# Kernel optimization log

Hardware: AMD Instinct MI355X
Metric: run time of the kernel (lower is better)

The kernel has to match this reference:

```python
import jax, jax.numpy as jnp
import numpy as np

HB, S, DK = 32, 2048, 128  # h*batch, seq_len, d_k
NEG = -1.0e9


def setup_inputs() -> dict:
    key = jax.random.key(0)
    kq, kk, kv = jax.random.split(key, 3)
    Q = jax.random.normal(kq, (HB, S, DK), dtype=jnp.float32)
    K = jax.random.normal(kk, (HB, S, DK), dtype=jnp.float32)
    V = jax.random.normal(kv, (HB, S, DK), dtype=jnp.float32)
    # causal mask, 1.0 where attending allowed, broadcast to all head*batch rows
    mask = jnp.broadcast_to(jnp.tril(jnp.ones((S, S), dtype=jnp.float32)), (HB, S, S))
    return {"Q": Q, "K": K, "V": V, "mask": mask}


def reference(Q, K, V, mask):
    d_k = Q.shape[-1]
    scores = jnp.einsum("bqd,bkd->bqk", Q, K) / jnp.sqrt(jnp.float32(d_k))
    scores = scores * mask + (1.0 - mask) * NEG
    p_attn = jax.nn.softmax(scores, axis=-1)
    # NOTE: original layer computes dropout(p_attn) but then discards it and
    # matmuls the un-dropped p_attn with V; we reproduce the inference math.
    out = jnp.einsum("bqk,bkd->bqd", p_attn, V)
    return (out, p_attn)
```

## Files before the change

kernel.cpp:

```cpp
#include <hip/hip_runtime.h>
#include <hip/hip_bf16.h>
#include <cstdint>

#define HB 32
#define SEQ 2048
#define DKDIM 128

typedef short s16x8 __attribute__((ext_vector_type(8)));
typedef float f32x4 __attribute__((ext_vector_type(4)));

__device__ __forceinline__ unsigned short f2bf(float x) {
  union { float f; uint32_t u; } v; v.f = x;
  uint32_t r = v.u + 0x7FFFu + ((v.u >> 16) & 1u);
  return (unsigned short)(r >> 16);
}
__device__ __forceinline__ float bf2f(unsigned short h) {
  union { uint32_t u; float f; } v; v.u = ((uint32_t)h) << 16;
  return v.f;
}

#define SCALE 0.08838834764831845f

__device__ __forceinline__ void barrier_lgkm_only() {
  asm volatile("s_waitcnt lgkmcnt(0)" ::: "memory");
  __builtin_amdgcn_s_barrier();
  __builtin_amdgcn_sched_barrier(0);
}

#define SK_KPAD 140
#define SK_KELEMS (64 * SK_KPAD)

__global__ __launch_bounds__(256, 4) void attn_sums(
    const float* __restrict__ Qg, const float* __restrict__ Kg, float* __restrict__ sums)
{
  __shared__ __align__(16) unsigned short K_lds[2 * SK_KELEMS];

  const int tid = threadIdx.x;
  const int lane = tid & 63;
  const int w = tid >> 6, g = lane >> 4, lr = lane & 15;
  const int b = blockIdx.y;
  const size_t bS = (size_t)b * SEQ;

  int x = blockIdx.x, qt = 0, acc = 0;
  for (;;) { int c = (qt >> 2) + 1; if (x < acc + c) break; acc += c; ++qt; }
  const int kc = x - acc;
  const int qb = qt << 6;
  const int t0 = kc << 2;
  const int nt = min(4, qt + 1 - t0);

  s16x8 qf[4];
  {
    const float* qrow = Qg + (bS + qb + w * 16 + lr) * DKDIM;
#pragma unroll
    for (int c = 0; c < 4; ++c) {
      const float* p = qrow + c * 32 + g * 8;
      float4 a = *(const float4*)p, bb = *(const float4*)(p + 4);
      s16x8 h;
      h[0] = (short)f2bf(a.x * SCALE); h[1] = (short)f2bf(a.y * SCALE);
      h[2] = (short)f2bf(a.z * SCALE); h[3] = (short)f2bf(a.w * SCALE);
      h[4] = (short)f2bf(bb.x * SCALE); h[5] = (short)f2bf(bb.y * SCALE);
      h[6] = (short)f2bf(bb.z * SCALE); h[7] = (short)f2bf(bb.w * SCALE);
      qf[c] = h;
    }
  }

  auto loadK = [&](int kt, float4* r) {
#pragma unroll
    for (int it = 0; it < 4; ++it) {
      int chunk = tid + (it << 8);
      const float* src = Kg + (bS + (kt << 6) + (chunk >> 4)) * (size_t)DKDIM + ((chunk & 15) << 3);
      r[2 * it] = *(const float4*)src;
      r[2 * it + 1] = *(const float4*)(src + 4);
    }
  };
  auto writeK = [&](unsigned short* dst, const float4* r) {
#pragma unroll
    for (int it = 0; it < 4; ++it) {
      int chunk = tid + (it << 8);
      int row = chunk >> 4, c8 = (chunk & 15) << 3;
      float4 a = r[2 * it], bb = r[2 * it + 1];
      s16x8 h;
      h[0] = (short)f2bf(a.x); h[1] = (short)f2bf(a.y); h[2] = (short)f2bf(a.z); h[3] = (short)f2bf(a.w);
      h[4] = (short)f2bf(bb.x); h[5] = (short)f2bf(bb.y); h[6] = (short)f2bf(bb.z); h[7] = (short)f2bf(bb.w);
      *(s16x8*)&dst[row * SK_KPAD + c8] = h;
    }
  };

  float4 kr[8];
  loadK(t0, kr);
  writeK(K_lds, kr);

  float rsum[4] = {0.f, 0.f, 0.f, 0.f};
  for (int j = 0; j < nt; ++j) {
    barrier_lgkm_only();
    const bool pf = (j + 1 < nt);
    if (pf) loadK(t0 + j + 1, kr);
    const unsigned short* Kb = K_lds + (j & 1) * SK_KELEMS;
    f32x4 sacc[4];
#pragma unroll
    for (int n = 0; n < 4; ++n) { f32x4 z = {0.f, 0.f, 0.f, 0.f}; sacc[n] = z; }
#pragma unroll
    for (int c = 0; c < 4; ++c)
#pragma unroll
      for (int n = 0; n < 4; ++n) {
        s16x8 bf = *(const s16x8*)&Kb[(n * 16 + lr) * SK_KPAD + (c << 5) + (g << 3)];
        sacc[n] = __builtin_amdgcn_mfma_f32_16x16x32_bf16(qf[c], bf, sacc[n], 0, 0, 0);
      }
    const int kt = t0 + j;
    if (kt == qt) {
#pragma unroll
      for (int n = 0; n < 4; ++n)
#pragma unroll
        for (int r = 0; r < 4; ++r) {
          const bool ok = ((kt << 6) + n * 16 + lr) <= (qb + w * 16 + g * 4 + r);
          rsum[r] += ok ? __expf(sacc[n][r]) : 0.0f;
        }
    } else {
#pragma unroll
      for (int n = 0; n < 4; ++n)
#pragma unroll
        for (int r = 0; r < 4; ++r) rsum[r] += __expf(sacc[n][r]);
    }
    if (pf) writeK(K_lds + ((j + 1) & 1) * SK_KELEMS, kr);
  }

#pragma unroll
  for (int r = 0; r < 4; ++r) {
    float v = rsum[r];
    v += __shfl_xor(v, 1, 64);
    v += __shfl_xor(v, 2, 64);
    v += __shfl_xor(v, 4, 64);
    v += __shfl_xor(v, 8, 64);
    rsum[r] = v;
  }
  if (lr == 0)
#pragma unroll
    for (int r = 0; r < 4; ++r)
      atomicAdd(&sums[bS + qb + w * 16 + g * 4 + r], rsum[r]);
}

#define M_KPAD 140
#define M_KELEMS (32 * M_KPAD)
#define M_VPAD 36
#define M_VELEMS (128 * M_VPAD)
#define M_PP 36

__global__ __launch_bounds__(256, 4) void attn_main(
    const float* __restrict__ Qg, const float* __restrict__ Kg, const float* __restrict__ Vg,
    const float* __restrict__ sums, float* __restrict__ outg, float* __restrict__ pg)
{
  __shared__ __align__(16) unsigned short smem[20480];

  const int tid = threadIdx.x;
  const int lane = tid & 63;
  const int w = tid >> 6, g = lane >> 4, lr = lane & 15;
  const int b = blockIdx.y;
  const int xx = blockIdx.x;
  const int qt = (xx & 1) ? (31 - (xx >> 1)) : (xx >> 1);
  const int qb = qt << 6;
  const size_t bS = (size_t)b * SEQ;
  const int nkt = (qt + 1) << 1;

  s16x8 qf[4];
  {
    const float* qrow = Qg + (bS + qb + w * 16 + lr) * DKDIM;
#pragma unroll
    for (int c = 0; c < 4; ++c) {
      const float* p = qrow + c * 32 + g * 8;
      float4 a = *(const float4*)p, bb = *(const float4*)(p + 4);
      s16x8 h;
      h[0] = (short)f2bf(a.x * SCALE); h[1] = (short)f2bf(a.y * SCALE);
      h[2] = (short)f2bf(a.z * SCALE); h[3] = (short)f2bf(a.w * SCALE);
      h[4] = (short)f2bf(bb.x * SCALE); h[5] = (short)f2bf(bb.y * SCALE);
      h[6] = (short)f2bf(bb.z * SCALE); h[7] = (short)f2bf(bb.w * SCALE);
      qf[c] = h;
    }
  }
  float inv[4];
#pragma unroll
  for (int r = 0; r < 4; ++r)
    inv[r] = 1.0f / sums[bS + qb + w * 16 + g * 4 + r];

  auto loadK = [&](int kt, float4* r) {
#pragma unroll
    for (int it = 0; it < 2; ++it) {
      int chunk = tid + (it << 8);
      const float* src = Kg + (bS + (kt << 5) + (chunk >> 4)) * (size_t)DKDIM + ((chunk & 15) << 3);
      r[2 * it] = *(const float4*)src;
      r[2 * it + 1] = *(const float4*)(src + 4);
    }
  };
  auto writeK = [&](unsigned short* dst, const float4* r) {
#pragma unroll
    for (int it = 0; it < 2; ++it) {
      int chunk = tid + (it << 8);
      int row = chunk >> 4, c8 = (chunk & 15) << 3;
      float4 a = r[2 * it], bb = r[2 * it + 1];
      s16x8 h;
      h[0] = (short)f2bf(a.x); h[1] = (short)f2bf(a.y); h[2] = (short)f2bf(a.z); h[3] = (short)f2bf(a.w);
      h[4] = (short)f2bf(bb.x); h[5] = (short)f2bf(bb.y); h[6] = (short)f2bf(bb.z); h[7] = (short)f2bf(bb.w);
      *(s16x8*)&dst[row * M_KPAD + c8] = h;
    }
  };
  auto loadV = [&](int kt, float4* r) {
    int row = tid & 31;
#pragma unroll
    for (int it = 0; it < 2; ++it) {
      int c8 = ((((tid >> 5) & 7) + (it << 3))) << 3;
      const float* src = Vg + (bS + (kt << 5) + row) * (size_t)DKDIM + c8;
      r[2 * it] = *(const float4*)src;
      r[2 * it + 1] = *(const float4*)(src + 4);
    }
  };
  auto writeV = [&](unsigned short* dst, const float4* r) {
    int row = tid & 31;
#pragma unroll
    for (int it = 0; it < 2; ++it) {
      int c8 = ((((tid >> 5) & 7) + (it << 3))) << 3;
      float4 a = r[2 * it], bb = r[2 * it + 1];
      float vv[8] = {a.x, a.y, a.z, a.w, bb.x, bb.y, bb.z, bb.w};
#pragma unroll
      for (int i = 0; i < 8; ++i) dst[(c8 + i) * M_VPAD + row] = f2bf(vv[i]);
    }
  };

  unsigned short* Pw = smem + 2 * M_KELEMS + 2 * M_VELEMS + w * 16 * M_PP;
  const int prow = lane >> 2;
  const int pc8 = (lane & 3) << 3;

  f32x4 oacc[8];
#pragma unroll
  for (int n = 0; n < 8; ++n) { f32x4 z = {0.f, 0.f, 0.f, 0.f}; oacc[n] = z; }

  float4 kr[4], vr[4];
  loadK(0, kr); loadV(0, vr);
  writeK(smem, kr); writeV(smem + 2 * M_KELEMS, vr);

  for (int kt = 0; kt < nkt; ++kt) {
    barrier_lgkm_only();
    const bool pf = (kt + 1 < nkt);
    if (pf) { loadK(kt + 1, kr); loadV(kt + 1, vr); }

    const unsigned short* Kb = smem + (kt & 1) * M_KELEMS;
    const unsigned short* Vb = smem + 2 * M_KELEMS + (kt & 1) * M_VELEMS;
    const int kb = kt << 5;

    f32x4 sacc[2];
    { f32x4 z = {0.f, 0.f, 0.f, 0.f}; sacc[0] = z; sacc[1] = z; }
#pragma unroll
    for (int c = 0; c < 4; ++c)
#pragma unroll
      for (int n = 0; n < 2; ++n) {
        s16x8 bf = *(const s16x8*)&Kb[(n * 16 + lr) * M_KPAD + (c << 5) + (g << 3)];
        sacc[n] = __builtin_amdgcn_mfma_f32_16x16x32_bf16(qf[c], bf, sacc[n], 0, 0, 0);
      }

    if (kb >= qb) {
#pragma unroll
      for (int n = 0; n < 2; ++n)
#pragma unroll
        for (int r = 0; r < 4; ++r) {
          const bool ok = (kb + n * 16 + lr) <= (qb + w * 16 + g * 4 + r);
          float e = ok ? __expf(sacc[n][r]) * inv[r] : 0.0f;
          Pw[(g * 4 + r) * M_PP + n * 16 + lr] = f2bf(e);
        }
    } else {
#pragma unroll
      for (int n = 0; n < 2; ++n)
#pragma unroll
        for (int r = 0; r < 4; ++r) {
          float e = __expf(sacc[n][r]) * inv[r];
          Pw[(g * 4 + r) * M_PP + n * 16 + lr] = f2bf(e);
        }
    }
    asm volatile("s_waitcnt lgkmcnt(0)" ::: "memory");

    {
      float* dst = pg + (bS + qb + w * 16 + prow) * SEQ + kb + pc8;
      s16x8 ph = *(const s16x8*)&Pw[prow * M_PP + pc8];
      float4 o;
      o.x = bf2f((unsigned short)ph[0]); o.y = bf2f((unsigned short)ph[1]);
      o.z = bf2f((unsigned short)ph[2]); o.w = bf2f((unsigned short)ph[3]);
      *(float4*)dst = o;
      o.x = bf2f((unsigned short)ph[4]); o.y = bf2f((unsigned short)ph[5]);
      o.z = bf2f((unsigned short)ph[6]); o.w = bf2f((unsigned short)ph[7]);
      *(float4*)(dst + 4) = o;
    }

    {
      s16x8 pa = *(const s16x8*)&Pw[lr * M_PP + (g << 3)];
#pragma unroll
      for (int n = 0; n < 8; ++n) {
        s16x8 vb = *(const s16x8*)&Vb[(n * 16 + lr) * M_VPAD + (g << 3)];
        oacc[n] = __builtin_amdgcn_mfma_f32_16x16x32_bf16(pa, vb, oacc[n], 0, 0, 0);
      }
    }

    if (pf) {
      writeK(smem + ((kt + 1) & 1) * M_KELEMS, kr);
      writeV(smem + 2 * M_KELEMS + ((kt + 1) & 1) * M_VELEMS, vr);
    }
  }

#pragma unroll
  for (int n = 0; n < 8; ++n)
#pragma unroll
    for (int r = 0; r < 4; ++r)
      outg[(bS + qb + w * 16 + g * 4 + r) * DKDIM + n * 16 + lr] = oacc[n][r];

  const int kcov = (qt + 1) << 6;
  if (kcov < SEQ) {
    f32x4 z = {0.f, 0.f, 0.f, 0.f};
    const int r0 = tid >> 4;
    const int cl = (tid & 15) << 2;
#pragma unroll
    for (int rr = r0; rr < 64; rr += 16) {
      float* prow_ = pg + (bS + qb + rr) * SEQ;
      for (int c = kcov + cl; c < SEQ; c += 64)
        *(f32x4*)(prow_ + c) = z;
    }
  }
}

extern "C" void kernel_launch(void* const* d_in, const int* in_sizes, int n_in,
                              void* d_out, int out_size, void* d_ws, size_t ws_size,
                              hipStream_t stream) {
  const float* Q = (const float*)d_in[0];
  const float* K = (const float*)d_in[1];
  const float* V = (const float*)d_in[2];
  float* out = (float*)d_out;
  float* p = out + (size_t)HB * SEQ * DKDIM;
  float* sums = (float*)d_ws;

  (void)hipMemsetAsync(sums, 0, (size_t)HB * SEQ * sizeof(float), stream);
  attn_sums<<<dim3(144, HB), 256, 0, stream>>>(Q, K, sums);
  attn_main<<<dim3(32, HB), 256, 0, stream>>>(Q, K, V, sums, out, p);
}
```

Before: 1.427 ms.

## Fuse QK recompute into single pass with unnormalized P and separate rescale kernel

```diff
diff --git a/kernel.cpp b/kernel.cpp
--- a/kernel.cpp
+++ b/kernel.cpp
@@ -27,13 +27,17 @@
   __builtin_amdgcn_sched_barrier(0);
 }
 
-#define SK_KPAD 140
-#define SK_KELEMS (64 * SK_KPAD)
-
-__global__ __launch_bounds__(256, 4) void attn_sums(
-    const float* __restrict__ Qg, const float* __restrict__ Kg, float* __restrict__ sums)
+#define KP 140
+#define KE (32 * KP)
+#define VP 36
+#define VE (128 * VP)
+#define PP 40
+
+__global__ __launch_bounds__(256, 4) void attn_pass1(
+    const float* __restrict__ Qg, const float* __restrict__ Kg, const float* __restrict__ Vg,
+    float* __restrict__ sums, float* __restrict__ outg, float* __restrict__ pg)
 {
-  __shared__ __align__(16) unsigned short K_lds[2 * SK_KELEMS];
+  __shared__ __align__(16) unsigned short smem[KE + VE + 4 * 16 * PP];
 
   const int tid = threadIdx.x;
   const int lane = tid & 63;
@@ -45,8 +49,8 @@
   for (;;) { int c = (qt >> 2) + 1; if (x < acc + c) break; acc += c; ++qt; }
   const int kc = x - acc;
   const int qb = qt << 6;
-  const int t0 = kc << 2;
-  const int nt = min(4, qt + 1 - t0);
+  const int t0 = kc << 3;
+  const int nt = min(8, 2 * (qt + 1) - t0);
 
   s16x8 qf[4];
   {
@@ -64,64 +68,98 @@
     }
   }
 
-  auto loadK = [&](int kt, float4* r) {
-#pragma unroll
-    for (int it = 0; it < 4; ++it) {
-      int chunk = tid + (it << 8);
-      const float* src = Kg + (bS + (kt << 6) + (chunk >> 4)) * (size_t)DKDIM + ((chunk & 15) << 3);
-      r[2 * it] = *(const float4*)src;
-      r[2 * it + 1] = *(const float4*)(src + 4);
-    }
-  };
-  auto writeK = [&](unsigned short* dst, const float4* r) {
-#pragma unroll
-    for (int it = 0; it < 4; ++it) {
+  unsigned short* Klds = smem;
+  unsigned short* Vlds = smem + KE;
+  unsigned short* Pw   = smem + KE + VE + w * 16 * PP;
+
+  float rsum[4] = {0.f, 0.f, 0.f, 0.f};
+  f32x4 oacc[8];
+#pragma unroll
+  for (int n = 0; n < 8; ++n) { f32x4 z = {0.f, 0.f, 0.f, 0.f}; oacc[n] = z; }
+
+  const int prow = lane >> 2;
+  const int pc8 = (lane & 3) << 3;
+
+  for (int j = 0; j < nt; ++j) {
+    const int kb = (t0 + j) << 5;
+    barrier_lgkm_only();
+#pragma unroll
+    for (int it = 0; it < 2; ++it) {
       int chunk = tid + (it << 8);
       int row = chunk >> 4, c8 = (chunk & 15) << 3;
-      float4 a = r[2 * it], bb = r[2 * it + 1];
+      const float* src = Kg + (bS + kb + row) * DKDIM + c8;
+      float4 a = *(const float4*)src, bb = *(const float4*)(src + 4);
       s16x8 h;
       h[0] = (short)f2bf(a.x); h[1] = (short)f2bf(a.y); h[2] = (short)f2bf(a.z); h[3] = (short)f2bf(a.w);
       h[4] = (short)f2bf(bb.x); h[5] = (short)f2bf(bb.y); h[6] = (short)f2bf(bb.z); h[7] = (short)f2bf(bb.w);
-      *(s16x8*)&dst[row * SK_KPAD + c8] = h;
-    }
-  };
-
-  float4 kr[8];
-  loadK(t0, kr);
-  writeK(K_lds, kr);
-
-  float rsum[4] = {0.f, 0.f, 0.f, 0.f};
-  for (int j = 0; j < nt; ++j) {
+      *(s16x8*)&Klds[row * KP + c8] = h;
+    }
+    {
+      int row = tid & 31;
+#pragma unroll
+      for (int it = 0; it < 2; ++it) {
+        int c8 = (((tid >> 5) & 7) + (it << 3)) << 3;
+        const float* src = Vg + (bS + kb + row) * DKDIM + c8;
+        float4 a = *(const float4*)src, bb = *(const float4*)(src + 4);
+        float vv[8] = {a.x, a.y, a.z, a.w, bb.x, bb.y, bb.z, bb.w};
+#pragma unroll
+        for (int i = 0; i < 8; ++i) Vlds[(c8 + i) * VP + row] = f2bf(vv[i]);
+      }
+    }
     barrier_lgkm_only();
-    const bool pf = (j + 1 < nt);
-    if (pf) loadK(t0 + j + 1, kr);
-    const unsigned short* Kb = K_lds + (j & 1) * SK_KELEMS;
-    f32x4 sacc[4];
-#pragma unroll
-    for (int n = 0; n < 4; ++n) { f32x4 z = {0.f, 0.f, 0.f, 0.f}; sacc[n] = z; }
+
+    f32x4 sacc[2];
+    { f32x4 z = {0.f, 0.f, 0.f, 0.f}; sacc[0] = z; sacc[1] = z; }
 #pragma unroll
     for (int c = 0; c < 4; ++c)
 #pragma unroll
-      for (int n = 0; n < 4; ++n) {
-        s16x8 bf = *(const s16x8*)&Kb[(n * 16 + lr) * SK_KPAD + (c << 5) + (g << 3)];
+      for (int n = 0; n < 2; ++n) {
+        s16x8 bf = *(const s16x8*)&Klds[(n * 16 + lr) * KP + (c << 5) + (g << 3)];
         sacc[n] = __builtin_amdgcn_mfma_f32_16x16x32_bf16(qf[c], bf, sacc[n], 0, 0, 0);
       }
-    const int kt = t0 + j;
-    if (kt == qt) {
-#pragma unroll
-      for (int n = 0; n < 4; ++n)
+
+    if (kb >= qb) {
+#pragma unroll
+      for (int n = 0; n < 2; ++n)
 #pragma unroll
         for (int r = 0; r < 4; ++r) {
-          const bool ok = ((kt << 6) + n * 16 + lr) <= (qb + w * 16 + g * 4 + r);
-          rsum[r] += ok ? __expf(sacc[n][r]) : 0.0f;
+          const bool ok = (kb + n * 16 + lr) <= (qb + w * 16 + g * 4 + r);
+          float e = ok ? __expf(sacc[n][r]) : 0.0f;
+          rsum[r] += e;
+          Pw[(g * 4 + r) * PP + n * 16 + lr] = f2bf(e);
         }
     } else {
 #pragma unroll
-      for (int n = 0; n < 4; ++n)
-#pragma unroll
-        for (int r = 0; r < 4; ++r) rsum[r] += __expf(sacc[n][r]);
-    }
-    if (pf) writeK(K_lds + ((j + 1) & 1) * SK_KELEMS, kr);
+      for (int n = 0; n < 2; ++n)
+#pragma unroll
+        for (int r = 0; r < 4; ++r) {
+          float e = __expf(sacc[n][r]);
+          rsum[r] += e;
+          Pw[(g * 4 + r) * PP + n * 16 + lr] = f2bf(e);
+        }
+    }
+    asm volatile("s_waitcnt lgkmcnt(0)" ::: "memory");
+
+    {
+      float* dst = pg + (bS + qb + w * 16 + prow) * SEQ + kb + pc8;
+      s16x8 ph = *(const s16x8*)&Pw[prow * PP + pc8];
+      float4 o;
+      o.x = bf2f((unsigned short)ph[0]); o.y = bf2f((unsigned short)ph[1]);
+      o.z = bf2f((unsigned short)ph[2]); o.w = bf2f((unsigned short)ph[3]);
+      *(float4*)dst = o;
+      o.x = bf2f((unsigned short)ph[4]); o.y = bf2f((unsigned short)ph[5]);
+      o.z = bf2f((unsigned short)ph[6]); o.w = bf2f((unsigned short)ph[7]);
+      *(float4*)(dst + 4) = o;
+    }
+
+    {
+      s16x8 pa = *(const s16x8*)&Pw[lr * PP + (g << 3)];
+#pragma unroll
+      for (int n = 0; n < 8; ++n) {
+        s16x8 vb = *(const s16x8*)&Vlds[(n * 16 + lr) * VP + (g << 3)];
+        oacc[n] = __builtin_amdgcn_mfma_f32_16x16x32_bf16(pa, vb, oacc[n], 0, 0, 0);
+      }
+    }
   }
 
 #pragma unroll
@@ -137,187 +175,46 @@
 #pragma unroll
     for (int r = 0; r < 4; ++r)
       atomicAdd(&sums[bS + qb + w * 16 + g * 4 + r], rsum[r]);
-}
-
-#define M_KPAD 140
-#define M_KELEMS (32 * M_KPAD)
-#define M_VPAD 36
-#define M_VELEMS (128 * M_VPAD)
-#define M_PP 36
-
-__global__ __launch_bounds__(256, 4) void attn_main(
-    const float* __restrict__ Qg, const float* __restrict__ Kg, const float* __restrict__ Vg,
-    const float* __restrict__ sums, float* __restrict__ outg, float* __restrict__ pg)
+
+#pragma unroll
+  for (int n = 0; n < 8; ++n)
+#pragma unroll
+    for (int r = 0; r < 4; ++r)
+      atomicAdd(&outg[(bS + qb + w * 16 + g * 4 + r) * DKDIM + n * 16 + lr], oacc[n][r]);
+}
+
+__global__ __launch_bounds__(256) void attn_scale(
+    float* __restrict__ pg, float* __restrict__ outg, const float* __restrict__ sums)
 {
-  __shared__ __align__(16) unsigned short smem[20480];
-
   const int tid = threadIdx.x;
-  const int lane = tid & 63;
-  const int w = tid >> 6, g = lane >> 4, lr = lane & 15;
-  const int b = blockIdx.y;
-  const int xx = blockIdx.x;
-  const int qt = (xx & 1) ? (31 - (xx >> 1)) : (xx >> 1);
-  const int qb = qt << 6;
-  const size_t bS = (size_t)b * SEQ;
-  const int nkt = (qt + 1) << 1;
-
-  s16x8 qf[4];
-  {
-    const float* qrow = Qg + (bS + qb + w * 16 + lr) * DKDIM;
-#pragma unroll
-    for (int c = 0; c < 4; ++c) {
-      const float* p = qrow + c * 32 + g * 8;
-      float4 a = *(const float4*)p, bb = *(const float4*)(p + 4);
-      s16x8 h;
-      h[0] = (short)f2bf(a.x * SCALE); h[1] = (short)f2bf(a.y * SCALE);
-      h[2] = (short)f2bf(a.z * SCALE); h[3] = (short)f2bf(a.w * SCALE);
-      h[4] = (short)f2bf(bb.x * SCALE); h[5] = (short)f2bf(bb.y * SCALE);
-      h[6] = (short)f2bf(bb.z * SCALE); h[7] = (short)f2bf(bb.w * SCALE);
-      qf[c] = h;
-    }
-  }
-  float inv[4];
-#pragma unroll
-  for (int r = 0; r < 4; ++r)
-    inv[r] = 1.0f / sums[bS + qb + w * 16 + g * 4 + r];
-
-  auto loadK = [&](int kt, float4* r) {
-#pragma unroll
-    for (int it = 0; it < 2; ++it) {
-      int chunk = tid + (it << 8);
-      const float* src = Kg + (bS + (kt << 5) + (chunk >> 4)) * (size_t)DKDIM + ((chunk & 15) << 3);
-      r[2 * it] = *(const float4*)src;
-      r[2 * it + 1] = *(const float4*)(src + 4);
-    }
-  };
-  auto writeK = [&](unsigned short* dst, const float4* r) {
-#pragma unroll
-    for (int it = 0; it < 2; ++it) {
-      int chunk = tid + (it << 8);
-      int row = chunk >> 4, c8 = (chunk & 15) << 3;
-      float4 a = r[2 * it], bb = r[2 * it + 1];
-      s16x8 h;
-      h[0] = (short)f2bf(a.x); h[1] = (short)f2bf(a.y); h[2] = (short)f2bf(a.z); h[3] = (short)f2bf(a.w);
-      h[4] = (short)f2bf(bb.x); h[5] = (short)f2bf(bb.y); h[6] = (short)f2bf(bb.z); h[7] = (short)f2bf(bb.w);
-      *(s16x8*)&dst[row * M_KPAD + c8] = h;
-    }
-  };
-  auto loadV = [&](int kt, float4* r) {
-    int row = tid & 31;
-#pragma unroll
-    for (int it = 0; it < 2; ++it) {
-      int c8 = ((((tid >> 5) & 7) + (it << 3))) << 3;
-      const float* src = Vg + (bS + (kt << 5) + row) * (size_t)DKDIM + c8;
-      r[2 * it] = *(const float4*)src;
-      r[2 * it + 1] = *(const float4*)(src + 4);
-    }
-  };
-  auto writeV = [&](unsigned short* dst, const float4* r) {
-    int row = tid & 31;
-#pragma unroll
-    for (int it = 0; it < 2; ++it) {
-      int c8 = ((((tid >> 5) & 7) + (it << 3))) << 3;
-      float4 a = r[2 * it], bb = r[2 * it + 1];
-      float vv[8] = {a.x, a.y, a.z, a.w, bb.x, bb.y, bb.z, bb.w};
-#pragma unroll
-      for (int i = 0; i < 8; ++i) dst[(c8 + i) * M_VPAD + row] = f2bf(vv[i]);
-    }
-  };
-
-  unsigned short* Pw = smem + 2 * M_KELEMS + 2 * M_VELEMS + w * 16 * M_PP;
-  const int prow = lane >> 2;
-  const int pc8 = (lane & 3) << 3;
-
-  f32x4 oacc[8];
-#pragma unroll
-  for (int n = 0; n < 8; ++n) { f32x4 z = {0.f, 0.f, 0.f, 0.f}; oacc[n] = z; }
-
-  float4 kr[4], vr[4];
-  loadK(0, kr); loadV(0, vr);
-  writeK(smem, kr); writeV(smem + 2 * M_KELEMS, vr);
-
-  for (int kt = 0; kt < nkt; ++kt) {
-    barrier_lgkm_only();
-    const bool pf = (kt + 1 < nkt);
-    if (pf) { loadK(kt + 1, kr); loadV(kt + 1, vr); }
-
-    const unsigned short* Kb = smem + (kt & 1) * M_KELEMS;
-    const unsigned short* Vb = smem + 2 * M_KELEMS + (kt & 1) * M_VELEMS;
-    const int kb = kt << 5;
-
-    f32x4 sacc[2];
-    { f32x4 z = {0.f, 0.f, 0.f, 0.f}; sacc[0] = z; sacc[1] = z; }
-#pragma unroll
-    for (int c = 0; c < 4; ++c)
-#pragma unroll
-      for (int n = 0; n < 2; ++n) {
-        s16x8 bf = *(const s16x8*)&Kb[(n * 16 + lr) * M_KPAD + (c << 5) + (g << 3)];
-        sacc[n] = __builtin_amdgcn_mfma_f32_16x16x32_bf16(qf[c], bf, sacc[n], 0, 0, 0);
-      }
-
-    if (kb >= qb) {
-#pragma unroll
-      for (int n = 0; n < 2; ++n)
-#pragma unroll
-        for (int r = 0; r < 4; ++r) {
-          const bool ok = (kb + n * 16 + lr) <= (qb + w * 16 + g * 4 + r);
-          float e = ok ? __expf(sacc[n][r]) * inv[r] : 0.0f;
-          Pw[(g * 4 + r) * M_PP + n * 16 + lr] = f2bf(e);
-        }
-    } else {
-#pragma unroll
-      for (int n = 0; n < 2; ++n)
-#pragma unroll
-        for (int r = 0; r < 4; ++r) {
-          float e = __expf(sacc[n][r]) * inv[r];
-          Pw[(g * 4 + r) * M_PP + n * 16 + lr] = f2bf(e);
-        }
-    }
-    asm volatile("s_waitcnt lgkmcnt(0)" ::: "memory");
-
-    {
-      float* dst = pg + (bS + qb + w * 16 + prow) * SEQ + kb + pc8;
-      s16x8 ph = *(const s16x8*)&Pw[prow * M_PP + pc8];
-      float4 o;
-      o.x = bf2f((unsigned short)ph[0]); o.y = bf2f((unsigned short)ph[1]);
-      o.z = bf2f((unsigned short)ph[2]); o.w = bf2f((unsigned short)ph[3]);
-      *(float4*)dst = o;
-      o.x = bf2f((unsigned short)ph[4]); o.y = bf2f((unsigned short)ph[5]);
-      o.z = bf2f((unsigned short)ph[6]); o.w = bf2f((unsigned short)ph[7]);
-      *(float4*)(dst + 4) = o;
-    }
-
-    {
-      s16x8 pa = *(const s16x8*)&Pw[lr * M_PP + (g << 3)];
-#pragma unroll
-      for (int n = 0; n < 8; ++n) {
-        s16x8 vb = *(const s16x8*)&Vb[(n * 16 + lr) * M_VPAD + (g << 3)];
-        oacc[n] = __builtin_amdgcn_mfma_f32_16x16x32_bf16(pa, vb, oacc[n], 0, 0, 0);
-      }
-    }
-
-    if (pf) {
-      writeK(smem + ((kt + 1) & 1) * M_KELEMS, kr);
-      writeV(smem + 2 * M_KELEMS + ((kt + 1) & 1) * M_VELEMS, vr);
-    }
-  }
-
-#pragma unroll
-  for (int n = 0; n < 8; ++n)
-#pragma unroll
-    for (int r = 0; r < 4; ++r)
-      outg[(bS + qb + w * 16 + g * 4 + r) * DKDIM + n * 16 + lr] = oacc[n][r];
-
-  const int kcov = (qt + 1) << 6;
-  if (kcov < SEQ) {
-    f32x4 z = {0.f, 0.f, 0.f, 0.f};
-    const int r0 = tid >> 4;
-    const int cl = (tid & 15) << 2;
-#pragma unroll
-    for (int rr = r0; rr < 64; rr += 16) {
-      float* prow_ = pg + (bS + qb + rr) * SEQ;
-      for (int c = kcov + cl; c < SEQ; c += 64)
-        *(f32x4*)(prow_ + c) = z;
+  const int bid = blockIdx.x;
+  if (bid < 16384) {
+    const int rowid = (bid << 2) + (tid >> 6);
+    const int lane = tid & 63;
+    const int q = rowid & (SEQ - 1);
+    const float inv = 1.0f / sums[rowid];
+    const int kcov4 = ((q & ~63) + 64) >> 2;
+    f32x4* prow = (f32x4*)pg + (size_t)rowid * (SEQ / 4);
+#pragma unroll
+    for (int i = 0; i < 8; ++i) {
+      const int c4 = lane + (i << 6);
+      if (c4 < kcov4) {
+        f32x4 v = prow[c4];
+        prow[c4] = v * inv;
+      } else {
+        f32x4 z = {0.f, 0.f, 0.f, 0.f};
+        prow[c4] = z;
+      }
+    }
+  } else {
+    const int k0 = (bid - 16384) << 12;
+    f32x4* o4 = (f32x4*)outg;
+#pragma unroll
+    for (int i = 0; i < 16; ++i) {
+      const int k = k0 + (i << 8) + tid;
+      const int rowid = k >> 5;
+      const float inv = 1.0f / sums[rowid];
+      o4[k] = o4[k] * inv;
     }
   }
 }
@@ -333,6 +230,7 @@
   float* sums = (float*)d_ws;
 
   (void)hipMemsetAsync(sums, 0, (size_t)HB * SEQ * sizeof(float), stream);
-  attn_sums<<<dim3(144, HB), 256, 0, stream>>>(Q, K, sums);
-  attn_main<<<dim3(32, HB), 256, 0, stream>>>(Q, K, V, sums, out, p);
-}
+  (void)hipMemsetAsync(out, 0, (size_t)HB * SEQ * DKDIM * sizeof(float), stream);
+  attn_pass1<<<dim3(144, HB), 256, 0, stream>>>(Q, K, V, sums, out, p);
+  attn_scale<<<16384 + 512, 256, 0, stream>>>(p, out, sums);
+}
```

Result: faster. 1.204 ms (-15.6%).
